# Kernel optimization log

Hardware: AMD Instinct MI355X
Metric: run time of the kernel (lower is better)

## Reference

```python
import jax, jax.numpy as jnp
import numpy as np

B, S, IN_DIM, HID, H, CS = 4, 4096, 1024, 1024, 16, 16
HD = HID // H
LN_EPS = 1e-5


def setup_inputs() -> dict:
    key = jax.random.key(0)
    ks = jax.random.split(key, 6)
    x = jax.random.normal(ks[0], (B, S, IN_DIM), jnp.float32)
    W_in = jax.random.normal(ks[1], (HID, IN_DIM), jnp.float32) * (IN_DIM ** -0.5)
    ln_g = jnp.ones((HID,), jnp.float32)
    ln_b = jnp.zeros((HID,), jnp.float32)
    W_gate = jax.random.normal(ks[2], (2 * H, HID), jnp.float32) * (HID ** -0.5)
    b_gate = jnp.zeros((2 * H,), jnp.float32)
    raw = 0.5 * float(np.log(1.9 / 0.1))  # atanh(0.9), as in _init_eigenvalues
    eig_raw = jnp.full((H,), raw, jnp.float32) + 0.01 * jax.random.normal(ks[3], (H,), jnp.float32)
    W_out = jax.random.normal(ks[4], (HID, HID), jnp.float32) * (HID ** -0.5)
    return {"x": x, "W_in": W_in, "ln_g": ln_g, "ln_b": ln_b,
            "W_gate": W_gate, "b_gate": b_gate, "eig_raw": eig_raw, "W_out": W_out}


def _chunk_scan(a, b):
    # a: (B,S,H) decay, b: (B,S,H,HD) input; h_t = a_t*h_{t-1} + b_t, h0 = 0
    Bsz, Sl = a.shape[0], a.shape[1]
    N = Sl // CS  # seq_len chosen divisible by chunk_size (pad_len == 0)
    ac = a.reshape(Bsz, N, CS, H)
    bc = b.reshape(Bsz, N, CS, H, HD)
    cum = jnp.cumprod(ac, axis=2)  # (B,N,C,H)
    ones = jnp.ones((Bsz, N, 1, H), a.dtype)
    cum_pad = jnp.concatenate([ones, cum[:, :, :-1]], axis=2)  # shifted cumprod
    # M[i,j] = cum_i / cum_pad_j for i>j, 1 on diag, 0 above
    Mi = cum[:, :, :, None, :]        # (B,N,C,1,H)
    Mj = cum_pad[:, :, None, :, :]    # (B,N,1,C,H)
    M = jnp.where(jnp.abs(Mj) > 1e-8, Mi / Mj, jnp.zeros_like(Mi))
    tril = jnp.tril(jnp.ones((CS, CS), a.dtype))[None, None, :, :, None]
    eye = jnp.eye(CS, dtype=a.dtype)[None, None, :, :, None]
    M = M * tril
    M = M * (1 - eye) + eye  # force exact 1 on diagonal
    # within-chunk contribution: (B,N,C,H,HD)
    h_contrib = jnp.einsum('bnijh,bnjhd->bnihd', M, bc)
    # inter-chunk sequential carry
    cum_T = jnp.moveaxis(cum, 1, 0)            # (N,B,C,H)
    hc_T = jnp.moveaxis(h_contrib, 1, 0)       # (N,B,C,H,HD)

    def step(h, inp):
        cum_n, hc_n = inp
        h_chunk = cum_n[..., None] * h[:, None] + hc_n  # (B,C,H,HD)
        return h_chunk[:, -1], h_chunk

    h0 = jnp.zeros((Bsz, H, HD), a.dtype)
    _, h_all = jax.lax.scan(step, h0, (cum_T, hc_T))   # (N,B,C,H,HD)
    h_all = jnp.moveaxis(h_all, 0, 1).reshape(Bsz, Sl, HID)
    return h_all


def reference(x, W_in, ln_g, ln_b, W_gate, b_gate, eig_raw, W_out):
    Bsz, Sl, _ = x.shape
    xp = x @ W_in.T                               # (B,S,HID)
    mu = jnp.mean(xp, axis=-1, keepdims=True)
    var = jnp.mean((xp - mu) ** 2, axis=-1, keepdims=True)
    xp = (xp - mu) * jax.lax.rsqrt(var + LN_EPS) * ln_g + ln_b
    gates = xp @ W_gate.T + b_gate                # (B,S,2H)
    alpha = jax.nn.sigmoid(gates[..., :H])
    beta = jax.nn.sigmoid(gates[..., H:])
    eig = jnp.tanh(eig_raw)                       # (H,)
    a = eig[None, None, :] * alpha                # (B,S,H)
    x_heads = xp.reshape(Bsz, Sl, H, HD)
    b = beta[..., None] * x_heads                 # (B,S,H,HD)
    h_all = _chunk_scan(a, b)                     # (B,S,HID)
    output = h_all @ W_out.T                      # dropout is identity in eval
    h_final = h_all[:, -1, :]
    return output, h_final
```

## Files before the change

kernel.cpp:

```cpp
#include <hip/hip_runtime.h>
#include <hip/hip_bf16.h>
#include <stdint.h>

#define BATCH 4
#define SEQ   4096
#define HID   1024
#define NH    16
#define HD    64
#define CS    16
#define NCH   256
#define MROWS 16384

typedef __attribute__((ext_vector_type(8))) __bf16 bf16x8;
typedef __attribute__((ext_vector_type(4))) float  f32x4;
typedef __attribute__((ext_vector_type(8))) unsigned short u16x8;

__device__ __forceinline__ unsigned short f2bf(float f) {
    union { float f; unsigned u; } x; x.f = f;
    unsigned r = x.u + 0x7FFFu + ((x.u >> 16) & 1u);
    return (unsigned short)(r >> 16);
}
__device__ __forceinline__ float bf2f(unsigned short v) {
    union { unsigned u; float f; } x; x.u = ((unsigned)v) << 16;
    return x.f;
}

__device__ __forceinline__ void async_copy16(void* lds, const void* g) {
    __builtin_amdgcn_global_load_lds(
        (const __attribute__((address_space(1))) unsigned int*)g,
        (__attribute__((address_space(3))) unsigned int*)lds,
        16, 0, 0);
}

__global__ __launch_bounds__(256) void convert_all_kernel(
    const float* __restrict__ x, const float* __restrict__ W_in,
    const float* __restrict__ W_out, const float* __restrict__ W_gate,
    unsigned short* __restrict__ xb, unsigned short* __restrict__ Wib,
    unsigned short* __restrict__ Wob, unsigned short* __restrict__ Wgb)
{
    int i = blockIdx.x * 256 + threadIdx.x;
    const float4* src; u16x8* dst; int j;
    if (i < 2097152)      { src = (const float4*)x;      dst = (u16x8*)xb;  j = i; }
    else if (i < 2228224) { src = (const float4*)W_in;   dst = (u16x8*)Wib; j = i - 2097152; }
    else if (i < 2359296) { src = (const float4*)W_out;  dst = (u16x8*)Wob; j = i - 2228224; }
    else if (i < 2363392) { src = (const float4*)W_gate; dst = (u16x8*)Wgb; j = i - 2359296; }
    else return;
    float4 a = src[2 * j], b = src[2 * j + 1];
    u16x8 o;
    o[0] = f2bf(a.x); o[1] = f2bf(a.y); o[2] = f2bf(a.z); o[3] = f2bf(a.w);
    o[4] = f2bf(b.x); o[5] = f2bf(b.y); o[6] = f2bf(b.z); o[7] = f2bf(b.w);
    dst[j] = o;
}

__global__ __launch_bounds__(256, 2) void gemm_bt_kernel(
    const unsigned short* __restrict__ A,
    const unsigned short* __restrict__ Bm,
    float* __restrict__ C, int M, int N, int K)
{
    __shared__ unsigned short As[128 * 64];
    __shared__ unsigned short Bs[128 * 64];
    const int t = threadIdx.x;
    const int lane = t & 63, w = t >> 6;
    const int wm = w >> 1, wn = w & 1;
    const size_t bm = (size_t)blockIdx.x * 128;
    const size_t bn = (size_t)blockIdx.y * 128;

    f32x4 acc[4][4];
#pragma unroll
    for (int x = 0; x < 4; x++)
#pragma unroll
        for (int y = 0; y < 4; y++)
            acc[x][y] = (f32x4){0.f, 0.f, 0.f, 0.f};

    const int srow = lane >> 3;
    const int gc   = (lane & 7) ^ (srow & 7);
    const int scol = gc * 8;
    const unsigned short* Ag = A + (bm + w * 32 + srow) * (size_t)K + scol;
    const unsigned short* Bg = Bm + (bn + w * 32 + srow) * (size_t)K + scol;
    unsigned short* Al = As + (w * 32 + srow) * 64 + (lane & 7) * 8;
    unsigned short* Bl = Bs + (w * 32 + srow) * 64 + (lane & 7) * 8;

    const int fr = lane & 15, fq = lane >> 4;
    const int rl = fr & 7;

    for (int k0 = 0; k0 < K; k0 += 64) {
#pragma unroll
        for (int r = 0; r < 4; r++) {
            async_copy16(Al + r * 8 * 64, Ag + (size_t)r * 8 * K + k0);
            async_copy16(Bl + r * 8 * 64, Bg + (size_t)r * 8 * K + k0);
        }
        __syncthreads();
#pragma unroll
        for (int kk = 0; kk < 64; kk += 32) {
            const int c = (kk >> 3) + fq;
            const int pc = c ^ rl;
            bf16x8 af[4], bfv[4];
#pragma unroll
            for (int x = 0; x < 4; x++) {
                af[x]  = *(const bf16x8*)(As + (wm * 64 + x * 16 + fr) * 64 + pc * 8);
                bfv[x] = *(const bf16x8*)(Bs + (wn * 64 + x * 16 + fr) * 64 + pc * 8);
            }
#pragma unroll
            for (int x = 0; x < 4; x++)
#pragma unroll
                for (int y = 0; y < 4; y++)
                    acc[x][y] = __builtin_amdgcn_mfma_f32_16x16x32_bf16(af[x], bfv[y], acc[x][y], 0, 0, 0);
        }
        __syncthreads();
    }

#pragma unroll
    for (int x = 0; x < 4; x++) {
#pragma unroll
        for (int y = 0; y < 4; y++) {
            size_t r0 = bm + wm * 64 + x * 16 + fq * 4;
            size_t c  = bn + wn * 64 + y * 16 + fr;
#pragma unroll
            for (int rg = 0; rg < 4; rg++)
                C[(r0 + rg) * (size_t)N + c] = acc[x][y][rg];
        }
    }
}

__global__ __launch_bounds__(256) void mid_kernel(
    const float* __restrict__ xp,
    const float* __restrict__ ln_g, const float* __restrict__ ln_b,
    const unsigned short* __restrict__ Wgb,
    const float* __restrict__ bg, const float* __restrict__ eig_raw,
    unsigned short* __restrict__ xln,
    float* __restrict__ beta_buf,
    float* __restrict__ cum_out,
    float* __restrict__ c15c,
    float* __restrict__ hc15)
{
    __shared__ unsigned short sx[16][1032];
    __shared__ float red[4][2][64][4];
    __shared__ float sg[16][32];
    __shared__ float scum[16][16];
    const int t = threadIdx.x, lane = t & 63, w = t >> 6;
    const int bn = blockIdx.x;
    const size_t m0 = (size_t)(bn >> 8) * SEQ + (size_t)(bn & 255) * 16;

    const int r = t >> 4, u = t & 15;
    {
        const float* row = xp + (m0 + r) * 1024;
        float4 va[8], vb[8];
        float s = 0.f, s2 = 0.f;
#pragma unroll
        for (int i = 0; i < 8; i++) {
            const int k = u * 8 + i * 128;
            va[i] = *(const float4*)(row + k);
            vb[i] = *(const float4*)(row + k + 4);
            s  += va[i].x + va[i].y + va[i].z + va[i].w
                + vb[i].x + vb[i].y + vb[i].z + vb[i].w;
            s2 += va[i].x * va[i].x + va[i].y * va[i].y + va[i].z * va[i].z + va[i].w * va[i].w
                + vb[i].x * vb[i].x + vb[i].y * vb[i].y + vb[i].z * vb[i].z + vb[i].w * vb[i].w;
        }
#pragma unroll
        for (int off = 1; off < 16; off <<= 1) {
            s  += __shfl_xor(s, off, 64);
            s2 += __shfl_xor(s2, off, 64);
        }
        const float mu = s * (1.f / 1024.f);
        const float var = s2 * (1.f / 1024.f) - mu * mu;
        const float sc = rsqrtf(var + 1e-5f);
        unsigned short* orow = xln + (m0 + r) * 1024;
#pragma unroll
        for (int i = 0; i < 8; i++) {
            const int k = u * 8 + i * 128;
            float4 g4a = *(const float4*)(ln_g + k);
            float4 g4b = *(const float4*)(ln_g + k + 4);
            float4 b4a = *(const float4*)(ln_b + k);
            float4 b4b = *(const float4*)(ln_b + k + 4);
            u16x8 o;
            o[0] = f2bf((va[i].x - mu) * sc * g4a.x + b4a.x);
            o[1] = f2bf((va[i].y - mu) * sc * g4a.y + b4a.y);
            o[2] = f2bf((va[i].z - mu) * sc * g4a.z + b4a.z);
            o[3] = f2bf((va[i].w - mu) * sc * g4a.w + b4a.w);
            o[4] = f2bf((vb[i].x - mu) * sc * g4b.x + b4b.x);
            o[5] = f2bf((vb[i].y - mu) * sc * g4b.y + b4b.y);
            o[6] = f2bf((vb[i].z - mu) * sc * g4b.z + b4b.z);
            o[7] = f2bf((vb[i].w - mu) * sc * g4b.w + b4b.w);
            *(u16x8*)&sx[r][k] = o;
            *(u16x8*)(orow + k) = o;
        }
    }
    __syncthreads();

    const int fr = lane & 15, fq = lane >> 4;
    {
        f32x4 acc0 = (f32x4){0.f,0.f,0.f,0.f}, acc1 = (f32x4){0.f,0.f,0.f,0.f};
        const unsigned short* Wr0 = Wgb + (size_t)fr * 1024;
        const unsigned short* Wr1 = Wgb + (size_t)(16 + fr) * 1024;
#pragma unroll
        for (int ks = 0; ks < 8; ks++) {
            const int k0 = w * 256 + ks * 32 + fq * 8;
            bf16x8 af = *(const bf16x8*)&sx[fr][k0];
            bf16x8 b0 = *(const bf16x8*)(Wr0 + k0);
            bf16x8 b1 = *(const bf16x8*)(Wr1 + k0);
            acc0 = __builtin_amdgcn_mfma_f32_16x16x32_bf16(af, b0, acc0, 0, 0, 0);
            acc1 = __builtin_amdgcn_mfma_f32_16x16x32_bf16(af, b1, acc1, 0, 0, 0);
        }
        *(f32x4*)&red[w][0][lane][0] = acc0;
        *(f32x4*)&red[w][1][lane][0] = acc1;
    }
    __syncthreads();
    if (t < 128) {
        const int y = t >> 6, l = t & 63;
        f32x4 s = *(const f32x4*)&red[0][y][l][0];
#pragma unroll
        for (int ww = 1; ww < 4; ww++) {
            f32x4 p = *(const f32x4*)&red[ww][y][l][0];
            s[0] += p[0]; s[1] += p[1]; s[2] += p[2]; s[3] += p[3];
        }
        const int col = y * 16 + (l & 15);
        const int row0 = (l >> 4) * 4;
        const float bias = bg[col];
#pragma unroll
        for (int rg = 0; rg < 4; rg++)
            sg[row0 + rg][col] = 1.f / (1.f + expf(-(s[rg] + bias)));
    }
    __syncthreads();

    if (t < 16) {
        const float ev = tanhf(eig_raw[t]);
        float c = 1.f;
#pragma unroll
        for (int i = 0; i < 16; i++) { c *= ev * sg[i][t]; scum[i][t] = c; }
    }
    beta_buf[(m0 + r) * 16 + u] = sg[r][16 + u];
    __syncthreads();

    cum_out[(size_t)bn * 256 + t] = scum[t >> 4][t & 15];
    if (t < 16) c15c[bn * 16 + t] = scum[15][t];

    {
        const int h = t >> 4, d0 = (t & 15) * 4;
        float s0 = 0.f, s1 = 0.f, s2 = 0.f, s3 = 0.f;
        float b0 = 0.f, b1 = 0.f, b2 = 0.f, b3 = 0.f;
        float cprev = 1.f;
#pragma unroll
        for (int j = 0; j < 16; j++) {
            const float bt = sg[j][16 + h];
            ushort4 xv = *(const ushort4*)&sx[j][h * 64 + d0];
            b0 = bt * bf2f(xv.x); b1 = bt * bf2f(xv.y);
            b2 = bt * bf2f(xv.z); b3 = bt * bf2f(xv.w);
            if (j < 15) {
                const float inv = (fabsf(cprev) > 1e-8f) ? (1.f / cprev) : 0.f;
                s0 += b0 * inv; s1 += b1 * inv; s2 += b2 * inv; s3 += b3 * inv;
                cprev = scum[j][h];
            }
        }
        const float c15 = scum[15][h];
        float4 o = { c15 * s0 + b0, c15 * s1 + b1, c15 * s2 + b2, c15 * s3 + b3 };
        *(float4*)(hc15 + (size_t)bn * 1024 + h * 64 + d0) = o;
    }
}

__global__ __launch_bounds__(256) void scan2a_kernel(
    const float* __restrict__ c15c,
    const float* __restrict__ hc15,
    float* __restrict__ Pg,
    float* __restrict__ Sg)
{
    const int tid = blockIdx.x * 256 + threadIdx.x;
    const int b = tid >> 14, g = (tid >> 10) & 15, hd = tid & 1023, h = hd >> 6;
    const int n0 = b * NCH + g * 16;
    float P = 1.f, S = 0.f;
#pragma unroll
    for (int j = 0; j < 16; j++) {
        const float c = c15c[(n0 + j) * 16 + h];
        S = c * S + hc15[(size_t)(n0 + j) * 1024 + hd];
        P = c * P;
    }
    Pg[tid] = P;
    Sg[tid] = S;
}

__global__ __launch_bounds__(256) void scan2c_kernel(
    const float* __restrict__ c15c, const float* __restrict__ hc15,
    const float* __restrict__ Pg, const float* __restrict__ Sg,
    float* __restrict__ carry_in,
    float* __restrict__ h_final)
{
    const int tid = blockIdx.x * 256 + threadIdx.x;
    const int b = tid >> 14, g = (tid >> 10) & 15, hd = tid & 1023, h = hd >> 6;
    const int n0 = b * NCH + g * 16;
    float s = 0.f;
    for (int gp = 0; gp < g; gp++) {
        const int idx = ((b * 16 + gp) << 10) + hd;
        s = Pg[idx] * s + Sg[idx];
    }
#pragma unroll
    for (int j = 0; j < 16; j++) {
        const size_t bn = n0 + j;
        carry_in[bn * 1024 + hd] = s;
        s = c15c[bn * 16 + h] * s + hc15[bn * 1024 + hd];
    }
    if (g == 15) h_final[(b << 10) + hd] = s;
}

__global__ __launch_bounds__(128) void scan3_kernel(
    const float* __restrict__ cum_buf,
    const float* __restrict__ beta_buf,
    const unsigned short* __restrict__ xln,
    const float* __restrict__ carry_in,
    unsigned short* __restrict__ hall)
{
    __shared__ float scum[16][16];
    __shared__ float sbeta[16][16];
    const int t = threadIdx.x;
    const int bn = blockIdx.x;
    const size_t m0 = (size_t)(bn >> 8) * SEQ + (size_t)(bn & 255) * 16;

    {
        const int i0 = t, i1 = t + 128;
        scum[i0 >> 4][i0 & 15]  = cum_buf[(size_t)bn * 256 + i0];
        scum[i1 >> 4][i1 & 15]  = cum_buf[(size_t)bn * 256 + i1];
        sbeta[i0 >> 4][i0 & 15] = beta_buf[(m0 + (i0 >> 4)) * 16 + (i0 & 15)];
        sbeta[i1 >> 4][i1 & 15] = beta_buf[(m0 + (i1 >> 4)) * 16 + (i1 & 15)];
    }
    __syncthreads();

    const int h = t >> 3, dq = t & 7;
    const size_t off = h * 64 + dq * 8;
    float s[8];
    *(float4*)&s[0] = *(const float4*)(carry_in + (size_t)bn * 1024 + off);
    *(float4*)&s[4] = *(const float4*)(carry_in + (size_t)bn * 1024 + off + 4);
    float cprev = 1.f;
#pragma unroll
    for (int i = 0; i < 16; i++) {
        u16x8 xv = *(const u16x8*)(xln + (m0 + i) * 1024 + off);
        const float bt = sbeta[i][h];
        const float ci = scum[i][h];
        float bb[8];
        u16x8 o;
#pragma unroll
        for (int e = 0; e < 8; e++) {
            bb[e] = bt * bf2f(xv[e]);
            o[e] = f2bf(ci * s[e] + bb[e]);
        }
        *(u16x8*)(hall + (m0 + i) * 1024 + off) = o;
        const float inv = (fabsf(cprev) > 1e-8f) ? (1.f / cprev) : 0.f;
#pragma unroll
        for (int e = 0; e < 8; e++)
            s[e] += bb[e] * inv;
        cprev = ci;
    }
}

extern "C" void kernel_launch(void* const* d_in, const int* in_sizes, int n_in,
                              void* d_out, int out_size, void* d_ws, size_t ws_size,
                              hipStream_t stream)
{
    const float* x       = (const float*)d_in[0];
    const float* W_in    = (const float*)d_in[1];
    const float* ln_g    = (const float*)d_in[2];
    const float* ln_b    = (const float*)d_in[3];
    const float* W_gate  = (const float*)d_in[4];
    const float* b_gate  = (const float*)d_in[5];
    const float* eig_raw = (const float*)d_in[6];
    const float* W_out   = (const float*)d_in[7];
    float* out = (float*)d_out;

    char* ws = (char*)d_ws;
    unsigned short* xb   = (unsigned short*)(ws);
    unsigned short* xln  = (unsigned short*)(ws);
    unsigned short* hall = (unsigned short*)(ws + 33554432);
    unsigned short* Wib  = (unsigned short*)(ws + 67108864);
    unsigned short* Wob  = (unsigned short*)(ws + 69206016);
    unsigned short* Wgb  = (unsigned short*)(ws + 71303168);
    float* beta_buf = (float*)(ws + 71368704);
    float* cum_buf  = (float*)(ws + 72417280);
    float* c15c     = (float*)(ws + 73465856);
    float* hc15     = (float*)(ws + 73531392);
    float* carry_in = (float*)(ws + 77725696);

    float* Pg = (float*)(ws + 33554432);
    float* Sg = (float*)(ws + 33554432 + 262144);

    float* xp = out;
    float* h_final = out + 16777216;

    convert_all_kernel<<<9232, 256, 0, stream>>>(x, W_in, W_out, W_gate, xb, Wib, Wob, Wgb);

    dim3 gg(128, 8);
    gemm_bt_kernel<<<gg, 256, 0, stream>>>(xb, Wib, xp, MROWS, HID, HID);

    mid_kernel<<<1024, 256, 0, stream>>>(xp, ln_g, ln_b, Wgb, b_gate, eig_raw,
                                         xln, beta_buf, cum_buf, c15c, hc15);

    scan2a_kernel<<<256, 256, 0, stream>>>(c15c, hc15, Pg, Sg);
    scan2c_kernel<<<256, 256, 0, stream>>>(c15c, hc15, Pg, Sg, carry_in, h_final);

    scan3_kernel<<<1024, 128, 0, stream>>>(cum_buf, beta_buf, xln, carry_in, hall);

    gemm_bt_kernel<<<gg, 256, 0, stream>>>(hall, Wob, out, MROWS, HID, HID);
}
```

Before: 253.5 us.

## Split layernorm out of mid kernel and fuse carry scan into scan3

Layernorm moves from the 1024-block mid kernel into its own 4096-block kernel with one wavefront per row, so that pass has more parallelism. The gate kernel then reads the bf16 normalized rows back from global memory. The scan2c kernel is removed: each scan3 block now rebuilds its incoming carry from the group prefix products and sums plus the chunk carries in its own group, and writes h_final itself. This saves a launch and the carry_in round trip, but adds redundant serial work per block and an extra bf16 read of xln.

```diff
diff --git a/kernel.cpp b/kernel.cpp
--- a/kernel.cpp
+++ b/kernel.cpp
@@ -122,12 +122,58 @@
     }
 }
 
-__global__ __launch_bounds__(256) void mid_kernel(
-    const float* __restrict__ xp,
-    const float* __restrict__ ln_g, const float* __restrict__ ln_b,
+__global__ __launch_bounds__(256) void ln_kernel(
+    const float* __restrict__ xp, const float* __restrict__ ln_g,
+    const float* __restrict__ ln_b, unsigned short* __restrict__ xln)
+{
+    const int row  = blockIdx.x * 4 + (threadIdx.x >> 6);
+    const int lane = threadIdx.x & 63;
+    const float* rp = xp + (size_t)row * 1024;
+    float4 va[2], vb[2];
+    float s = 0.f, s2 = 0.f;
+#pragma unroll
+    for (int i = 0; i < 2; i++) {
+        const int k = lane * 8 + i * 512;
+        va[i] = *(const float4*)(rp + k);
+        vb[i] = *(const float4*)(rp + k + 4);
+        s  += va[i].x + va[i].y + va[i].z + va[i].w
+            + vb[i].x + vb[i].y + vb[i].z + vb[i].w;
+        s2 += va[i].x * va[i].x + va[i].y * va[i].y + va[i].z * va[i].z + va[i].w * va[i].w
+            + vb[i].x * vb[i].x + vb[i].y * vb[i].y + vb[i].z * vb[i].z + vb[i].w * vb[i].w;
+    }
+#pragma unroll
+    for (int off = 1; off < 64; off <<= 1) {
+        s  += __shfl_xor(s, off, 64);
+        s2 += __shfl_xor(s2, off, 64);
+    }
+    const float mu  = s * (1.f / 1024.f);
+    const float var = s2 * (1.f / 1024.f) - mu * mu;
+    const float sc  = rsqrtf(var + 1e-5f);
+    unsigned short* orow = xln + (size_t)row * 1024;
+#pragma unroll
+    for (int i = 0; i < 2; i++) {
+        const int k = lane * 8 + i * 512;
+        float4 g4a = *(const float4*)(ln_g + k);
+        float4 g4b = *(const float4*)(ln_g + k + 4);
+        float4 b4a = *(const float4*)(ln_b + k);
+        float4 b4b = *(const float4*)(ln_b + k + 4);
+        u16x8 o;
+        o[0] = f2bf((va[i].x - mu) * sc * g4a.x + b4a.x);
+        o[1] = f2bf((va[i].y - mu) * sc * g4a.y + b4a.y);
+        o[2] = f2bf((va[i].z - mu) * sc * g4a.z + b4a.z);
+        o[3] = f2bf((va[i].w - mu) * sc * g4a.w + b4a.w);
+        o[4] = f2bf((vb[i].x - mu) * sc * g4b.x + b4b.x);
+        o[5] = f2bf((vb[i].y - mu) * sc * g4b.y + b4b.y);
+        o[6] = f2bf((vb[i].z - mu) * sc * g4b.z + b4b.z);
+        o[7] = f2bf((vb[i].w - mu) * sc * g4b.w + b4b.w);
+        *(u16x8*)(orow + k) = o;
+    }
+}
+
+__global__ __launch_bounds__(256) void gates_kernel(
+    const unsigned short* __restrict__ xln,
     const unsigned short* __restrict__ Wgb,
     const float* __restrict__ bg, const float* __restrict__ eig_raw,
-    unsigned short* __restrict__ xln,
     float* __restrict__ beta_buf,
     float* __restrict__ cum_out,
     float* __restrict__ c15c,
@@ -140,49 +186,14 @@
     const int t = threadIdx.x, lane = t & 63, w = t >> 6;
     const int bn = blockIdx.x;
     const size_t m0 = (size_t)(bn >> 8) * SEQ + (size_t)(bn & 255) * 16;
-
     const int r = t >> 4, u = t & 15;
+
     {
-        const float* row = xp + (m0 + r) * 1024;
-        float4 va[8], vb[8];
-        float s = 0.f, s2 = 0.f;
+        const unsigned short* xrow = xln + (m0 + r) * 1024;
 #pragma unroll
         for (int i = 0; i < 8; i++) {
             const int k = u * 8 + i * 128;
-            va[i] = *(const float4*)(row + k);
-            vb[i] = *(const float4*)(row + k + 4);
-            s  += va[i].x + va[i].y + va[i].z + va[i].w
-                + vb[i].x + vb[i].y + vb[i].z + vb[i].w;
-            s2 += va[i].x * va[i].x + va[i].y * va[i].y + va[i].z * va[i].z + va[i].w * va[i].w
-                + vb[i].x * vb[i].x + vb[i].y * vb[i].y + vb[i].z * vb[i].z + vb[i].w * vb[i].w;
-        }
-#pragma unroll
-        for (int off = 1; off < 16; off <<= 1) {
-            s  += __shfl_xor(s, off, 64);
-            s2 += __shfl_xor(s2, off, 64);
-        }
-        const float mu = s * (1.f / 1024.f);
-        const float var = s2 * (1.f / 1024.f) - mu * mu;
-        const float sc = rsqrtf(var + 1e-5f);
-        unsigned short* orow = xln + (m0 + r) * 1024;
-#pragma unroll
-        for (int i = 0; i < 8; i++) {
-            const int k = u * 8 + i * 128;
-            float4 g4a = *(const float4*)(ln_g + k);
-            float4 g4b = *(const float4*)(ln_g + k + 4);
-            float4 b4a = *(const float4*)(ln_b + k);
-            float4 b4b = *(const float4*)(ln_b + k + 4);
-            u16x8 o;
-            o[0] = f2bf((va[i].x - mu) * sc * g4a.x + b4a.x);
-            o[1] = f2bf((va[i].y - mu) * sc * g4a.y + b4a.y);
-            o[2] = f2bf((va[i].z - mu) * sc * g4a.z + b4a.z);
-            o[3] = f2bf((va[i].w - mu) * sc * g4a.w + b4a.w);
-            o[4] = f2bf((vb[i].x - mu) * sc * g4b.x + b4b.x);
-            o[5] = f2bf((vb[i].y - mu) * sc * g4b.y + b4b.y);
-            o[6] = f2bf((vb[i].z - mu) * sc * g4b.z + b4b.z);
-            o[7] = f2bf((vb[i].w - mu) * sc * g4b.w + b4b.w);
-            *(u16x8*)&sx[r][k] = o;
-            *(u16x8*)(orow + k) = o;
+            *(u16x8*)&sx[r][k] = *(const u16x8*)(xrow + k);
         }
     }
     __syncthreads();
@@ -277,41 +288,23 @@
     Sg[tid] = S;
 }
 
-__global__ __launch_bounds__(256) void scan2c_kernel(
-    const float* __restrict__ c15c, const float* __restrict__ hc15,
-    const float* __restrict__ Pg, const float* __restrict__ Sg,
-    float* __restrict__ carry_in,
-    float* __restrict__ h_final)
-{
-    const int tid = blockIdx.x * 256 + threadIdx.x;
-    const int b = tid >> 14, g = (tid >> 10) & 15, hd = tid & 1023, h = hd >> 6;
-    const int n0 = b * NCH + g * 16;
-    float s = 0.f;
-    for (int gp = 0; gp < g; gp++) {
-        const int idx = ((b * 16 + gp) << 10) + hd;
-        s = Pg[idx] * s + Sg[idx];
-    }
-#pragma unroll
-    for (int j = 0; j < 16; j++) {
-        const size_t bn = n0 + j;
-        carry_in[bn * 1024 + hd] = s;
-        s = c15c[bn * 16 + h] * s + hc15[bn * 1024 + hd];
-    }
-    if (g == 15) h_final[(b << 10) + hd] = s;
-}
-
 __global__ __launch_bounds__(128) void scan3_kernel(
     const float* __restrict__ cum_buf,
     const float* __restrict__ beta_buf,
     const unsigned short* __restrict__ xln,
-    const float* __restrict__ carry_in,
-    unsigned short* __restrict__ hall)
+    const float* __restrict__ c15c,
+    const float* __restrict__ hc15,
+    const float* __restrict__ Pg,
+    const float* __restrict__ Sg,
+    unsigned short* __restrict__ hall,
+    float* __restrict__ h_final)
 {
     __shared__ float scum[16][16];
     __shared__ float sbeta[16][16];
     const int t = threadIdx.x;
     const int bn = blockIdx.x;
-    const size_t m0 = (size_t)(bn >> 8) * SEQ + (size_t)(bn & 255) * 16;
+    const int b = bn >> 8, n = bn & 255, g = n >> 4;
+    const size_t m0 = (size_t)b * SEQ + (size_t)n * 16;
 
     {
         const int i0 = t, i1 = t + 128;
@@ -324,9 +317,40 @@
 
     const int h = t >> 3, dq = t & 7;
     const size_t off = h * 64 + dq * 8;
+
     float s[8];
-    *(float4*)&s[0] = *(const float4*)(carry_in + (size_t)bn * 1024 + off);
-    *(float4*)&s[4] = *(const float4*)(carry_in + (size_t)bn * 1024 + off + 4);
+#pragma unroll
+    for (int e = 0; e < 8; e++) s[e] = 0.f;
+    for (int gp = 0; gp < g; gp++) {
+        const size_t idx = ((size_t)(b * 16 + gp) << 10) + off;
+        float4 p0 = *(const float4*)(Pg + idx), p1 = *(const float4*)(Pg + idx + 4);
+        float4 q0 = *(const float4*)(Sg + idx), q1 = *(const float4*)(Sg + idx + 4);
+        s[0] = p0.x * s[0] + q0.x; s[1] = p0.y * s[1] + q0.y;
+        s[2] = p0.z * s[2] + q0.z; s[3] = p0.w * s[3] + q0.w;
+        s[4] = p1.x * s[4] + q1.x; s[5] = p1.y * s[5] + q1.y;
+        s[6] = p1.z * s[6] + q1.z; s[7] = p1.w * s[7] + q1.w;
+    }
+    for (int jj = (g << 4); jj < n; jj++) {
+        const size_t cn = (size_t)b * 256 + jj;
+        const float c = c15c[cn * 16 + h];
+        float4 h0 = *(const float4*)(hc15 + cn * 1024 + off);
+        float4 h1 = *(const float4*)(hc15 + cn * 1024 + off + 4);
+        s[0] = c * s[0] + h0.x; s[1] = c * s[1] + h0.y;
+        s[2] = c * s[2] + h0.z; s[3] = c * s[3] + h0.w;
+        s[4] = c * s[4] + h1.x; s[5] = c * s[5] + h1.y;
+        s[6] = c * s[6] + h1.z; s[7] = c * s[7] + h1.w;
+    }
+    if (n == 255) {
+        const size_t cn = (size_t)b * 256 + 255;
+        const float c = c15c[cn * 16 + h];
+        float4 h0 = *(const float4*)(hc15 + cn * 1024 + off);
+        float4 h1 = *(const float4*)(hc15 + cn * 1024 + off + 4);
+        float4 f0 = { c * s[0] + h0.x, c * s[1] + h0.y, c * s[2] + h0.z, c * s[3] + h0.w };
+        float4 f1 = { c * s[4] + h1.x, c * s[5] + h1.y, c * s[6] + h1.z, c * s[7] + h1.w };
+        *(float4*)(h_final + ((size_t)b << 10) + off)     = f0;
+        *(float4*)(h_final + ((size_t)b << 10) + off + 4) = f1;
+    }
+
     float cprev = 1.f;
 #pragma unroll
     for (int i = 0; i < 16; i++) {
@@ -374,10 +398,8 @@
     float* cum_buf  = (float*)(ws + 72417280);
     float* c15c     = (float*)(ws + 73465856);
     float* hc15     = (float*)(ws + 73531392);
-    float* carry_in = (float*)(ws + 77725696);
-
-    float* Pg = (float*)(ws + 33554432);
-    float* Sg = (float*)(ws + 33554432 + 262144);
+    float* Pg = (float*)(ws + 77725696);
+    float* Sg = (float*)(ws + 77725696 + 262144);
 
     float* xp = out;
     float* h_final = out + 16777216;
@@ -387,13 +409,15 @@
     dim3 gg(128, 8);
     gemm_bt_kernel<<<gg, 256, 0, stream>>>(xb, Wib, xp, MROWS, HID, HID);
 
-    mid_kernel<<<1024, 256, 0, stream>>>(xp, ln_g, ln_b, Wgb, b_gate, eig_raw,
-                                         xln, beta_buf, cum_buf, c15c, hc15);
+    ln_kernel<<<4096, 256, 0, stream>>>(xp, ln_g, ln_b, xln);
+
+    gates_kernel<<<1024, 256, 0, stream>>>(xln, Wgb, b_gate, eig_raw,
+                                           beta_buf, cum_buf, c15c, hc15);
 
     scan2a_kernel<<<256, 256, 0, stream>>>(c15c, hc15, Pg, Sg);
-    scan2c_kernel<<<256, 256, 0, stream>>>(c15c, hc15, Pg, Sg, carry_in, h_final);
-
-    scan3_kernel<<<1024, 128, 0, stream>>>(cum_buf, beta_buf, xln, carry_in, hall);
+
+    scan3_kernel<<<1024, 128, 0, stream>>>(cum_buf, beta_buf, xln, c15c, hc15,
+                                           Pg, Sg, hall, h_final);
 
     gemm_bt_kernel<<<gg, 256, 0, stream>>>(hall, Wob, out, MROWS, HID, HID);
 }
```

Result: no change. 254.3 us (+0.3%).
